# Kernel optimization log

Measured on AMD Instinct MI355X. Metric: run time of the kernel, lower is better.

Reference implementation:

```python
import math
import jax, jax.numpy as jnp
import numpy as np

B, N, D = 32, 1025, 768
K, CD, TD = 64, 128, 256  # num_clusters, cluster_dim, token_dim
REG = 0.1
NUM_ITERS = 5


def setup_inputs() -> dict:
    key = jax.random.key(0)
    ks = jax.random.split(key, 8)
    x = jax.random.normal(ks[0], (B, N, D), dtype=jnp.float32)
    # Linear params (torch nn.Linear: y = x @ W.T + b; we store W already transposed as [in, out])
    Wf = jax.random.normal(ks[1], (D, CD), dtype=jnp.float32) / math.sqrt(D)
    bf = jnp.zeros((CD,), dtype=jnp.float32)
    Ws = jax.random.normal(ks[2], (D, K), dtype=jnp.float32) / math.sqrt(D)
    bs = jnp.zeros((K,), dtype=jnp.float32)
    Wt = jax.random.normal(ks[3], (D, TD), dtype=jnp.float32) / math.sqrt(D)
    bt = jnp.zeros((TD,), dtype=jnp.float32)
    anchors = jax.random.normal(ks[4], (K, CD), dtype=jnp.float32) * 0.1
    dust_bin = jnp.float32(1.0)
    sharpness = jnp.float32(5.0)
    return {"x": x, "Wf": Wf, "bf": bf, "Ws": Ws, "bs": bs, "Wt": Wt, "bt": bt,
            "anchors": anchors, "dust_bin": dust_bin, "sharpness": sharpness}


def _log_otp_solver(log_a, log_b, M, num_iters, reg):
    M = M / reg
    u = jnp.zeros_like(log_a)  # [B, K+1]
    v = jnp.zeros_like(log_b)  # [B, N-1]
    for _ in range(num_iters):
        u = log_a - jax.nn.logsumexp(M + v[:, None, :], axis=2)
        v = log_b - jax.nn.logsumexp(M + u[:, :, None], axis=1)
    return M + u[:, :, None] + v[:, None, :]


def reference(x, Wf, bf, Ws, bs, Wt, bt, anchors, dust_bin, sharpness):
    b, n, d = x.shape
    t_global = x[:, 0]            # [B, D]
    fi = x[:, 1:]                 # [B, N-1, D]
    f = fi @ Wf + bf              # [B, N-1, CD]
    s = jnp.swapaxes(fi @ Ws + bs, 1, 2)  # [B, K, N-1]
    t = t_global @ Wt + bt        # [B, TD]
    s = s * sharpness
    dust = jnp.broadcast_to(dust_bin, (b, 1, n - 1))
    s_aug = jnp.concatenate([s, dust], axis=1)  # [B, K+1, N-1]
    log_a = jnp.full((b, K + 1), -math.log(K + 1), dtype=x.dtype)
    log_b = jnp.full((b, n - 1), -math.log(n - 1), dtype=x.dtype)
    log_P = _log_otp_solver(log_a, log_b, s_aug, NUM_ITERS, REG)
    p = jnp.exp(log_P)[:, :-1, :]  # [B, K, N-1]
    # v_agg = sum_n p[b,k,n] * (2*f[b,n,:] - anchors[k,:])  (algebraic rewrite of the broadcast sum)
    v_agg = 2.0 * jnp.einsum('bkn,bnc->bkc', p, f) - p.sum(axis=2)[:, :, None] * anchors[None]
    v_local = v_agg.reshape(b, -1)            # [B, K*CD]
    f_out = jnp.concatenate([t, v_local], axis=-1)
    norm = jnp.maximum(jnp.linalg.norm(f_out, axis=-1, keepdims=True), 1e-12)
    return f_out / norm
```

## Files before the change

### kernel.cpp

```cpp
#include <hip/hip_runtime.h>
#include <math.h>


#define BATCH 32
#define NTOK  1025
#define DIM   768
#define KDIM  64
#define CDIM  128
#define TDIM  256
#define NM1   1024
#define ROWLEN 8448
#define NITER 5
#define INV_REG 10.0f
#define NS_AGG 8
#define LOG_A (-4.17438727f)
#define LOG_B (-6.93147181f)

typedef __attribute__((ext_vector_type(8))) short short8;
typedef __attribute__((ext_vector_type(4))) float floatx4;

typedef __attribute__((address_space(3))) unsigned int lds_uint;
typedef const __attribute__((address_space(1))) unsigned int glb_uint;

__device__ __forceinline__ void gload_lds16(const void* g, void* l) {
    __builtin_amdgcn_global_load_lds((glb_uint*)g, (lds_uint*)l, 16, 0, 0);
}

__device__ __forceinline__ unsigned short bf16_rne(float f) {
    unsigned u = __builtin_bit_cast(unsigned, f);
    unsigned r = u + 0x7FFFu + ((u >> 16) & 1u);
    return (unsigned short)(r >> 16);
}

__device__ __forceinline__ short8 cvt8(float4 a, float4 b) {
    short8 r;
    r[0] = (short)bf16_rne(a.x); r[1] = (short)bf16_rne(a.y);
    r[2] = (short)bf16_rne(a.z); r[3] = (short)bf16_rne(a.w);
    r[4] = (short)bf16_rne(b.x); r[5] = (short)bf16_rne(b.y);
    r[6] = (short)bf16_rne(b.z); r[7] = (short)bf16_rne(b.w);
    return r;
}

__global__ __launch_bounds__(256) void prep(
    const float* __restrict__ Wf, const float* __restrict__ Ws,
    const float* __restrict__ bf, const float* __restrict__ bs,
    const float* __restrict__ x, const float* __restrict__ Wt,
    short* __restrict__ W_pack, float* __restrict__ bias_all,
    float* __restrict__ tpart)
{
    __shared__ float xr[256];
    const int blk = blockIdx.x, tid = threadIdx.x;
    if (blk < 576) {
        int idx = blk * 256 + tid;
        int g    = idx / 6144;
        int rem  = idx - g * 6144;
        int nf   = rem >> 9;
        int rem2 = rem & 511;
        int lane = rem2 >> 3;
        int j    = rem2 & 7;
        int k = g * 32 + (lane >> 4) * 8 + j;
        int c = nf * 16 + (lane & 15);
        float v = (c < CDIM) ? Wf[(size_t)k * CDIM + c] : Ws[(size_t)k * KDIM + (c - CDIM)];
        W_pack[idx] = (short)bf16_rne(v);
        if (idx < 192) bias_all[idx] = (idx < CDIM) ? bf[idx] : bs[idx - CDIM];
    } else {
        int i = blk - 576;
        int b = i / 3, dy = i - b * 3;
        xr[tid] = x[(size_t)b * NTOK * DIM + (size_t)dy * 256 + tid];
        __syncthreads();
        float acc = 0.f;
        const float* wp = Wt + (size_t)dy * 256 * TDIM + tid;
#pragma unroll 8
        for (int d = 0; d < 256; ++d) acc = fmaf(xr[d], wp[(size_t)d * TDIM], acc);
        tpart[((size_t)dy * BATCH + b) * TDIM + tid] = acc;
    }
}

__global__ __launch_bounds__(256, 2) void gemm_fs(
    const float* __restrict__ x, const short* __restrict__ W_pack,
    const float* __restrict__ bias_all, const float* __restrict__ sharp_p,
    unsigned short* __restrict__ fT, float* __restrict__ Mmat)
{
    __shared__ __align__(16) short Bs[12288];
    __shared__ __align__(16) short As[4096];
    const int tid  = threadIdx.x;
    const int wave = tid >> 6, lane = tid & 63;
    const int quad = lane >> 4, lrow = lane & 15;
    const int bb0   = blockIdx.x & 31;
    const int chunk = blockIdx.x >> 5;
    const int R = bb0 * 1024 + chunk * 64 + wave * 16;

    const int arow = bb0 * 1024 + chunk * 64 + (tid >> 2);
    const float* asrc = x + ((size_t)(arow >> 10) * NTOK + 1 + (arow & 1023)) * DIM + (tid & 3) * 16;
    const int r    = (tid >> 2) & 15;
    const int seg  = tid & 3;
    const int kk_w = seg >> 1;
    const int q0   = (seg & 1) * 2;
    short* adst0 = &As[(((tid >> 6) * 2 + kk_w) * 64 + q0 * 16 + r) * 8];
    short* adst1 = &As[(((tid >> 6) * 2 + kk_w) * 64 + (q0 + 1) * 16 + r) * 8];

    floatx4 acc[12];
#pragma unroll
    for (int nf = 0; nf < 12; ++nf) acc[nf] = (floatx4){0.f, 0.f, 0.f, 0.f};

    float4 g0 = *(const float4*)(asrc);
    float4 g1 = *(const float4*)(asrc + 4);
    float4 g2 = *(const float4*)(asrc + 8);
    float4 g3 = *(const float4*)(asrc + 12);

    for (int ko = 0; ko < 12; ++ko) {
        __syncthreads();
        const short* bsrc = W_pack + ko * 12288 + tid * 8;
#pragma unroll
        for (int i = 0; i < 6; ++i)
            gload_lds16(bsrc + i * 2048, &Bs[i * 2048 + tid * 8]);
        *(short8*)adst0 = cvt8(g0, g1);
        *(short8*)adst1 = cvt8(g2, g3);
        if (ko < 11) {
            const float* ap = asrc + (ko + 1) * 64;
            g0 = *(const float4*)(ap);
            g1 = *(const float4*)(ap + 4);
            g2 = *(const float4*)(ap + 8);
            g3 = *(const float4*)(ap + 12);
        }
        __syncthreads();
#pragma unroll
        for (int kk = 0; kk < 2; ++kk) {
            short8 af = *(const short8*)&As[((wave * 2 + kk) * 64 + lane) * 8];
#pragma unroll
            for (int nf = 0; nf < 12; ++nf) {
                short8 bf8 = *(const short8*)&Bs[((kk * 12 + nf) * 64 + lane) * 8];
                acc[nf] = __builtin_amdgcn_mfma_f32_16x16x32_bf16(af, bf8, acc[nf], 0, 0, 0);
            }
        }
    }

    const float sc = sharp_p[0] * INV_REG;
    const int bb = R >> 10;
    const int tok = (R & 1023) + quad * 4;
#pragma unroll
    for (int nf = 0; nf < 12; ++nf) {
        const int c = nf * 16 + lrow;
        const float bias = bias_all[c];
        if (nf < 8) {
            ushort4 w;
            w.x = bf16_rne(acc[nf][0] + bias);
            w.y = bf16_rne(acc[nf][1] + bias);
            w.z = bf16_rne(acc[nf][2] + bias);
            w.w = bf16_rne(acc[nf][3] + bias);
            *(ushort4*)(fT + ((size_t)bb * CDIM + c) * NM1 + tok) = w;
        } else {
            const int k = c - CDIM;
            float4 w = make_float4((acc[nf][0] + bias) * sc, (acc[nf][1] + bias) * sc,
                                   (acc[nf][2] + bias) * sc, (acc[nf][3] + bias) * sc);
            *(float4*)(Mmat + ((size_t)bb * KDIM + k) * NM1 + tok) = w;
        }
    }
}

template<bool FIRST>
__global__ __launch_bounds__(256) void sink_u(
    const float* __restrict__ Mmat, const float* __restrict__ v_in,
    const float* __restrict__ dust_p, float* __restrict__ u_out)
{
    const int b   = blockIdx.x & 31;
    const int sub = blockIdx.x >> 5;
    const int k   = sub * 4 + (threadIdx.x >> 6);
    if (k > 64) return;
    const int lane = threadIdx.x & 63;
    const float dustM = dust_p[0] * INV_REG;

    const float4* vp = (const float4*)(v_in + (size_t)b * NM1);
    float xs[16];
    if (k < 64) {
        const float4* Mp = (const float4*)(Mmat + ((size_t)b * KDIM + k) * NM1);
#pragma unroll
        for (int i = 0; i < 4; ++i) {
            float4 mv = Mp[i * 64 + lane];
            float4 vv = FIRST ? make_float4(0.f, 0.f, 0.f, 0.f) : vp[i * 64 + lane];
            xs[i * 4 + 0] = mv.x + vv.x;
            xs[i * 4 + 1] = mv.y + vv.y;
            xs[i * 4 + 2] = mv.z + vv.z;
            xs[i * 4 + 3] = mv.w + vv.w;
        }
    } else {
#pragma unroll
        for (int i = 0; i < 4; ++i) {
            float4 vv = FIRST ? make_float4(0.f, 0.f, 0.f, 0.f) : vp[i * 64 + lane];
            xs[i * 4 + 0] = dustM + vv.x;
            xs[i * 4 + 1] = dustM + vv.y;
            xs[i * 4 + 2] = dustM + vv.z;
            xs[i * 4 + 3] = dustM + vv.w;
        }
    }
    float m = xs[0];
#pragma unroll
    for (int i = 1; i < 16; ++i) m = fmaxf(m, xs[i]);
#pragma unroll
    for (int off = 1; off < 64; off <<= 1) m = fmaxf(m, __shfl_xor(m, off));
    float S = 0.f;
#pragma unroll
    for (int i = 0; i < 16; ++i) S += __expf(xs[i] - m);
#pragma unroll
    for (int off = 1; off < 64; off <<= 1) S += __shfl_xor(S, off);
    if (lane == 0) u_out[b * 65 + k] = LOG_A - (m + __logf(S));
}

__global__ __launch_bounds__(256) void sink_v(
    const float* __restrict__ Mmat, const float* __restrict__ u_in,
    const float* __restrict__ dust_p, float* __restrict__ v_out)
{
    __shared__ float us[65];
    __shared__ float2 pp[4][64];
    const int b   = blockIdx.x & 31;
    const int ns2 = blockIdx.x >> 5;
    const int tid = threadIdx.x;
    const int tok = tid & 63, kq = tid >> 6;
    const int n = ns2 * 64 + tok;
    if (tid < 65) us[tid] = u_in[b * 65 + tid];
    __syncthreads();
    const float* Mb = Mmat + ((size_t)b * KDIM + kq * 16) * NM1 + n;
    float xs[16];
#pragma unroll
    for (int kk = 0; kk < 16; ++kk) xs[kk] = Mb[(size_t)kk * NM1] + us[kq * 16 + kk];
    float m = xs[0];
#pragma unroll
    for (int kk = 1; kk < 16; ++kk) m = fmaxf(m, xs[kk]);
    float e = 0.f;
#pragma unroll
    for (int kk = 0; kk < 16; ++kk) e += __expf(xs[kk] - m);
    pp[kq][tok] = make_float2(m, e);
    __syncthreads();
    if (tid < 64) {
        const float xd = dust_p[0] * INV_REG + us[64];
        float m3 = xd;
#pragma unroll
        for (int q = 0; q < 4; ++q) m3 = fmaxf(m3, pp[q][tid].x);
        float S3 = __expf(xd - m3);
#pragma unroll
        for (int q = 0; q < 4; ++q) S3 += pp[q][tid].y * __expf(pp[q][tid].x - m3);
        v_out[(size_t)b * NM1 + ns2 * 64 + tid] = LOG_B - (m3 + __logf(S3));
    }
}

__global__ __launch_bounds__(256) void aggregate(
    const float* __restrict__ Mmat, const unsigned short* __restrict__ fT,
    const float* __restrict__ u_in, const float* __restrict__ dust_p,
    float* __restrict__ vpart, float* __restrict__ rspart)
{
    __shared__ float us[65];
    __shared__ __align__(16) float vsh[128];
    __shared__ float wv[4][128][2];
    const int b = blockIdx.x, ns = blockIdx.y;
    const int tid = threadIdx.x;
    const int wave = tid >> 6, lane = tid & 63;
    const int quad = lane >> 4, lrow = lane & 15;
    const int krow = wave * 16 + lrow;
    const float dustM = dust_p[0] * INV_REG;

    if (tid < 65) us[tid] = u_in[b * 65 + tid];
    __syncthreads();

    float mreg[32];
    {
        const float* Mrow = Mmat + ((size_t)b * KDIM + krow) * NM1 + ns * 128 + quad * 8;
#pragma unroll
        for (int s = 0; s < 4; ++s) {
            float4 a = *(const float4*)(Mrow + s * 32);
            float4 c = *(const float4*)(Mrow + s * 32 + 4);
            mreg[s*8+0]=a.x; mreg[s*8+1]=a.y; mreg[s*8+2]=a.z; mreg[s*8+3]=a.w;
            mreg[s*8+4]=c.x; mreg[s*8+5]=c.y; mreg[s*8+6]=c.z; mreg[s*8+7]=c.w;
        }
    }

    const float uk = us[krow];
#pragma unroll
    for (int s = 0; s < 4; ++s) {
#pragma unroll
        for (int j = 0; j < 8; ++j) {
            float x = mreg[s*8+j] + uk;
            float m2 = x;
            m2 = fmaxf(m2, __shfl_xor(m2, 1));
            m2 = fmaxf(m2, __shfl_xor(m2, 2));
            m2 = fmaxf(m2, __shfl_xor(m2, 4));
            m2 = fmaxf(m2, __shfl_xor(m2, 8));
            float e = __expf(x - m2);
            e += __shfl_xor(e, 1);
            e += __shfl_xor(e, 2);
            e += __shfl_xor(e, 4);
            e += __shfl_xor(e, 8);
            if (lrow == 0) {
                wv[wave][s*32 + quad*8 + j][0] = m2;
                wv[wave][s*32 + quad*8 + j][1] = e;
            }
        }
    }
    __syncthreads();
    if (tid < 128) {
        const float xd = dustM + us[64];
        float m3 = xd;
#pragma unroll
        for (int w = 0; w < 4; ++w) m3 = fmaxf(m3, wv[w][tid][0]);
        float S3 = __expf(xd - m3);
#pragma unroll
        for (int w = 0; w < 4; ++w) S3 += wv[w][tid][1] * __expf(wv[w][tid][0] - m3);
        vsh[tid] = LOG_B - (m3 + __logf(S3));
    }
    __syncthreads();

    const unsigned short* fbase = fT + ((size_t)b * CDIM + lrow) * NM1 + ns * 128 + quad * 8;
    floatx4 acc[8];
#pragma unroll
    for (int nf = 0; nf < 8; ++nf) acc[nf] = (floatx4){0.f, 0.f, 0.f, 0.f};
    float rs = 0.f;
#pragma unroll
    for (int s = 0; s < 4; ++s) {
        const int tb = s * 32 + quad * 8;
        float4 v0 = *(const float4*)&vsh[tb];
        float4 v1 = *(const float4*)&vsh[tb + 4];
        float p[8];
        p[0] = __expf(mreg[s*8+0] + uk + v0.x);
        p[1] = __expf(mreg[s*8+1] + uk + v0.y);
        p[2] = __expf(mreg[s*8+2] + uk + v0.z);
        p[3] = __expf(mreg[s*8+3] + uk + v0.w);
        p[4] = __expf(mreg[s*8+4] + uk + v1.x);
        p[5] = __expf(mreg[s*8+5] + uk + v1.y);
        p[6] = __expf(mreg[s*8+6] + uk + v1.z);
        p[7] = __expf(mreg[s*8+7] + uk + v1.w);
        short8 afrag;
#pragma unroll
        for (int j = 0; j < 8; ++j) {
            rs += p[j];
            afrag[j] = (short)bf16_rne(p[j]);
        }
#pragma unroll
        for (int nf = 0; nf < 8; ++nf) {
            short8 bfrag = *(const short8*)(fbase + (size_t)nf * 16 * NM1 + s * 32);
            acc[nf] = __builtin_amdgcn_mfma_f32_16x16x32_bf16(afrag, bfrag, acc[nf], 0, 0, 0);
        }
    }
    rs += __shfl_xor(rs, 16);
    rs += __shfl_xor(rs, 32);
    if (lane < 16) rspart[(ns * BATCH + b) * KDIM + krow] = rs;

    float* vp = vpart + (size_t)(ns * BATCH + b) * (KDIM * CDIM);
#pragma unroll
    for (int nf = 0; nf < 8; ++nf) {
        const int c = nf * 16 + lrow;
#pragma unroll
        for (int j = 0; j < 4; ++j)
            vp[(size_t)(wave * 16 + quad * 4 + j) * CDIM + c] = acc[nf][j];
    }
}

__global__ __launch_bounds__(1024) void finalize_all(
    const float* __restrict__ vpart, const float* __restrict__ rspart,
    const float* __restrict__ anchors, const float* __restrict__ tpart,
    const float* __restrict__ bt, float* __restrict__ out)
{
    __shared__ float rstot[KDIM];
    __shared__ float red[16];
    __shared__ float sc_sh;
    const int b = blockIdx.x, tid = threadIdx.x;
    const int lane = tid & 63, wave = tid >> 6;

    if (tid < KDIM) {
        float s = 0.f;
#pragma unroll
        for (int ns = 0; ns < NS_AGG; ++ns)
            s += rspart[(ns * BATCH + b) * KDIM + tid];
        rstot[tid] = s;
    }
    __syncthreads();

    const size_t e0 = (size_t)tid * 8;
    float4 s0 = make_float4(0.f, 0.f, 0.f, 0.f);
    float4 s1 = make_float4(0.f, 0.f, 0.f, 0.f);
#pragma unroll
    for (int ns = 0; ns < NS_AGG; ++ns) {
        const float* vp = vpart + (size_t)(ns * BATCH + b) * (KDIM * CDIM) + e0;
        float4 a = *(const float4*)(vp);
        float4 c = *(const float4*)(vp + 4);
        s0.x += a.x; s0.y += a.y; s0.z += a.z; s0.w += a.w;
        s1.x += c.x; s1.y += c.y; s1.z += c.z; s1.w += c.w;
    }
    const float rsv = rstot[tid >> 4];
    float4 a0 = *(const float4*)(anchors + e0);
    float4 a1 = *(const float4*)(anchors + e0 + 4);
    float4 v0, v1;
    v0.x = 2.f * s0.x - rsv * a0.x;  v0.y = 2.f * s0.y - rsv * a0.y;
    v0.z = 2.f * s0.z - rsv * a0.z;  v0.w = 2.f * s0.w - rsv * a0.w;
    v1.x = 2.f * s1.x - rsv * a1.x;  v1.y = 2.f * s1.y - rsv * a1.y;
    v1.z = 2.f * s1.z - rsv * a1.z;  v1.w = 2.f * s1.w - rsv * a1.w;
    float ss = v0.x*v0.x + v0.y*v0.y + v0.z*v0.z + v0.w*v0.w
             + v1.x*v1.x + v1.y*v1.y + v1.z*v1.z + v1.w*v1.w;

    float t = 0.f;
    if (tid < TDIM) {
        t = bt[tid];
#pragma unroll
        for (int s = 0; s < 3; ++s) t += tpart[((size_t)s * BATCH + b) * TDIM + tid];
        ss += t * t;
    }

#pragma unroll
    for (int off = 32; off > 0; off >>= 1) ss += __shfl_down(ss, off);
    if (lane == 0) red[wave] = ss;
    __syncthreads();
    if (tid == 0) {
        float tot = 0.f;
#pragma unroll
        for (int i = 0; i < 16; ++i) tot += red[i];
        sc_sh = 1.f / fmaxf(sqrtf(tot), 1e-12f);
    }
    __syncthreads();
    const float scale = sc_sh;

    float* orow = out + (size_t)b * ROWLEN;
    if (tid < TDIM) orow[tid] = t * scale;
    v0.x *= scale; v0.y *= scale; v0.z *= scale; v0.w *= scale;
    v1.x *= scale; v1.y *= scale; v1.z *= scale; v1.w *= scale;
    *(float4*)&orow[TDIM + e0]     = v0;
    *(float4*)&orow[TDIM + e0 + 4] = v1;
}

extern "C" void kernel_launch(void* const* d_in, const int* in_sizes, int n_in,
                              void* d_out, int out_size, void* d_ws, size_t ws_size,
                              hipStream_t stream)
{
    const float* x       = (const float*)d_in[0];
    const float* Wf      = (const float*)d_in[1];
    const float* bf      = (const float*)d_in[2];
    const float* Ws      = (const float*)d_in[3];
    const float* bs      = (const float*)d_in[4];
    const float* Wt      = (const float*)d_in[5];
    const float* bt      = (const float*)d_in[6];
    const float* anchors = (const float*)d_in[7];
    const float* dust    = (const float*)d_in[8];
    const float* sharp   = (const float*)d_in[9];
    float* out = (float*)d_out;

    char* base = (char*)d_ws;
    short* W_pack        = (short*)base;
    float* bias_all      = (float*)(base + 294912);
    float* Mmat          = bias_all + 192;
    unsigned short* fT   = (unsigned short*)(Mmat + (size_t)BATCH * KDIM * NM1);
    float* u_buf         = (float*)(fT + (size_t)BATCH * CDIM * NM1);
    float* v_buf         = u_buf + BATCH * 65;
    float* vpart         = v_buf + BATCH * NM1;
    float* rspart        = vpart + (size_t)NS_AGG * BATCH * KDIM * CDIM;
    float* tpart         = rspart + NS_AGG * BATCH * KDIM;

    hipLaunchKernelGGL(prep, dim3(672), dim3(256), 0, stream,
                       Wf, Ws, bf, bs, x, Wt, W_pack, bias_all, tpart);
    hipLaunchKernelGGL(gemm_fs, dim3(512), dim3(256), 0, stream,
                       x, W_pack, bias_all, sharp, fT, Mmat);

    hipLaunchKernelGGL(HIP_KERNEL_NAME(sink_u<true>), dim3(544), dim3(256), 0, stream,
                       Mmat, v_buf, dust, u_buf);
    for (int it = 1; it < NITER; ++it) {
        hipLaunchKernelGGL(sink_v, dim3(512), dim3(256), 0, stream,
                           Mmat, u_buf, dust, v_buf);
        hipLaunchKernelGGL(HIP_KERNEL_NAME(sink_u<false>), dim3(544), dim3(256), 0, stream,
                           Mmat, v_buf, dust, u_buf);
    }

    hipLaunchKernelGGL(aggregate, dim3(BATCH, NS_AGG), dim3(256), 0, stream,
                       Mmat, fT, u_buf, dust, vpart, rspart);
    hipLaunchKernelGGL(finalize_all, dim3(BATCH), dim3(1024), 0, stream,
                       vpart, rspart, anchors, tpart, bt, out);
}
```

Before: 245.5 us.

## Fuse Sinkhorn u/v half-steps into split-reduction kernels with partial logsumexp

Replaces the alternating sink_u/sink_v kernels with a single sink_uv kernel per iteration. Each block computes v for its token slice and then emits partial (max, sum) pairs for the next u update, and the consumer combines them. The first u partials are produced in the gemm_fs epilogue, and aggregate now merges the final partials itself. This cuts the launch count from about 10 to 4 plus aggregate and avoids re-reading Mmat twice per iteration. The cost is some extra reduction work, and it relies on a correct partial-logsumexp merge that treats the dust row specially.

```diff
diff --git a/kernel.cpp b/kernel.cpp
--- a/kernel.cpp
+++ b/kernel.cpp
@@ -79,10 +79,12 @@
 __global__ __launch_bounds__(256, 2) void gemm_fs(
     const float* __restrict__ x, const short* __restrict__ W_pack,
     const float* __restrict__ bias_all, const float* __restrict__ sharp_p,
-    unsigned short* __restrict__ fT, float* __restrict__ Mmat)
+    unsigned short* __restrict__ fT, float* __restrict__ Mmat,
+    float2* __restrict__ part0)
 {
     __shared__ __align__(16) short Bs[12288];
     __shared__ __align__(16) short As[4096];
+    __shared__ float2 sm[4][4][16];
     const int tid  = threadIdx.x;
     const int wave = tid >> 6, lane = tid & 63;
     const int quad = lane >> 4, lrow = lane & 15;
@@ -154,113 +156,50 @@
             float4 w = make_float4((acc[nf][0] + bias) * sc, (acc[nf][1] + bias) * sc,
                                    (acc[nf][2] + bias) * sc, (acc[nf][3] + bias) * sc);
             *(float4*)(Mmat + ((size_t)bb * KDIM + k) * NM1 + tok) = w;
-        }
-    }
-}
-
-template<bool FIRST>
-__global__ __launch_bounds__(256) void sink_u(
-    const float* __restrict__ Mmat, const float* __restrict__ v_in,
-    const float* __restrict__ dust_p, float* __restrict__ u_out)
-{
-    const int b   = blockIdx.x & 31;
-    const int sub = blockIdx.x >> 5;
-    const int k   = sub * 4 + (threadIdx.x >> 6);
-    if (k > 64) return;
-    const int lane = threadIdx.x & 63;
-    const float dustM = dust_p[0] * INV_REG;
-
-    const float4* vp = (const float4*)(v_in + (size_t)b * NM1);
-    float xs[16];
-    if (k < 64) {
-        const float4* Mp = (const float4*)(Mmat + ((size_t)b * KDIM + k) * NM1);
-#pragma unroll
-        for (int i = 0; i < 4; ++i) {
-            float4 mv = Mp[i * 64 + lane];
-            float4 vv = FIRST ? make_float4(0.f, 0.f, 0.f, 0.f) : vp[i * 64 + lane];
-            xs[i * 4 + 0] = mv.x + vv.x;
-            xs[i * 4 + 1] = mv.y + vv.y;
-            xs[i * 4 + 2] = mv.z + vv.z;
-            xs[i * 4 + 3] = mv.w + vv.w;
-        }
-    } else {
-#pragma unroll
-        for (int i = 0; i < 4; ++i) {
-            float4 vv = FIRST ? make_float4(0.f, 0.f, 0.f, 0.f) : vp[i * 64 + lane];
-            xs[i * 4 + 0] = dustM + vv.x;
-            xs[i * 4 + 1] = dustM + vv.y;
-            xs[i * 4 + 2] = dustM + vv.z;
-            xs[i * 4 + 3] = dustM + vv.w;
-        }
-    }
-    float m = xs[0];
-#pragma unroll
-    for (int i = 1; i < 16; ++i) m = fmaxf(m, xs[i]);
-#pragma unroll
-    for (int off = 1; off < 64; off <<= 1) m = fmaxf(m, __shfl_xor(m, off));
-    float S = 0.f;
-#pragma unroll
-    for (int i = 0; i < 16; ++i) S += __expf(xs[i] - m);
-#pragma unroll
-    for (int off = 1; off < 64; off <<= 1) S += __shfl_xor(S, off);
-    if (lane == 0) u_out[b * 65 + k] = LOG_A - (m + __logf(S));
-}
-
-__global__ __launch_bounds__(256) void sink_v(
-    const float* __restrict__ Mmat, const float* __restrict__ u_in,
-    const float* __restrict__ dust_p, float* __restrict__ v_out)
-{
-    __shared__ float us[65];
-    __shared__ float2 pp[4][64];
-    const int b   = blockIdx.x & 31;
-    const int ns2 = blockIdx.x >> 5;
-    const int tid = threadIdx.x;
-    const int tok = tid & 63, kq = tid >> 6;
-    const int n = ns2 * 64 + tok;
-    if (tid < 65) us[tid] = u_in[b * 65 + tid];
-    __syncthreads();
-    const float* Mb = Mmat + ((size_t)b * KDIM + kq * 16) * NM1 + n;
-    float xs[16];
-#pragma unroll
-    for (int kk = 0; kk < 16; ++kk) xs[kk] = Mb[(size_t)kk * NM1] + us[kq * 16 + kk];
-    float m = xs[0];
-#pragma unroll
-    for (int kk = 1; kk < 16; ++kk) m = fmaxf(m, xs[kk]);
-    float e = 0.f;
-#pragma unroll
-    for (int kk = 0; kk < 16; ++kk) e += __expf(xs[kk] - m);
-    pp[kq][tok] = make_float2(m, e);
-    __syncthreads();
-    if (tid < 64) {
-        const float xd = dust_p[0] * INV_REG + us[64];
-        float m3 = xd;
-#pragma unroll
-        for (int q = 0; q < 4; ++q) m3 = fmaxf(m3, pp[q][tid].x);
-        float S3 = __expf(xd - m3);
-#pragma unroll
-        for (int q = 0; q < 4; ++q) S3 += pp[q][tid].y * __expf(pp[q][tid].x - m3);
-        v_out[(size_t)b * NM1 + ns2 * 64 + tid] = LOG_B - (m3 + __logf(S3));
-    }
-}
-
-__global__ __launch_bounds__(256) void aggregate(
-    const float* __restrict__ Mmat, const unsigned short* __restrict__ fT,
-    const float* __restrict__ u_in, const float* __restrict__ dust_p,
-    float* __restrict__ vpart, float* __restrict__ rspart)
+            float m = fmaxf(fmaxf(w.x, w.y), fmaxf(w.z, w.w));
+            m = fmaxf(m, __shfl_xor(m, 16));
+            m = fmaxf(m, __shfl_xor(m, 32));
+            float e = __expf(w.x - m) + __expf(w.y - m)
+                    + __expf(w.z - m) + __expf(w.w - m);
+            e += __shfl_xor(e, 16);
+            e += __shfl_xor(e, 32);
+            if (quad == 0) sm[wave][nf - 8][lrow] = make_float2(m, e);
+        }
+    }
+    __syncthreads();
+    if (tid < 65) {
+        float2 o;
+        if (tid < 64) {
+            float2 p0 = sm[0][tid >> 4][tid & 15];
+            float2 p1 = sm[1][tid >> 4][tid & 15];
+            float2 p2 = sm[2][tid >> 4][tid & 15];
+            float2 p3 = sm[3][tid >> 4][tid & 15];
+            float m = fmaxf(fmaxf(p0.x, p1.x), fmaxf(p2.x, p3.x));
+            float e = p0.y * __expf(p0.x - m) + p1.y * __expf(p1.x - m)
+                    + p2.y * __expf(p2.x - m) + p3.y * __expf(p3.x - m);
+            o = make_float2(m, e);
+        } else {
+            o = make_float2(0.f, 64.f);
+        }
+        part0[((size_t)bb0 * 16 + chunk) * 65 + tid] = o;
+    }
+}
+
+template<int NSIN>
+__global__ __launch_bounds__(256) void sink_uv(
+    const float* __restrict__ Mmat, const float* __restrict__ dust_p,
+    const float2* __restrict__ pin, float2* __restrict__ pout)
 {
     __shared__ float us[65];
     __shared__ __align__(16) float vsh[128];
     __shared__ float wv[4][128][2];
-    const int b = blockIdx.x, ns = blockIdx.y;
+    const int b = blockIdx.x & 31, ns = blockIdx.x >> 5;
     const int tid = threadIdx.x;
     const int wave = tid >> 6, lane = tid & 63;
     const int quad = lane >> 4, lrow = lane & 15;
     const int krow = wave * 16 + lrow;
     const float dustM = dust_p[0] * INV_REG;
 
-    if (tid < 65) us[tid] = u_in[b * 65 + tid];
-    __syncthreads();
-
     float mreg[32];
     {
         const float* Mrow = Mmat + ((size_t)b * KDIM + krow) * NM1 + ns * 128 + quad * 8;
@@ -272,6 +211,19 @@
             mreg[s*8+4]=c.x; mreg[s*8+5]=c.y; mreg[s*8+6]=c.z; mreg[s*8+7]=c.w;
         }
     }
+
+    if (tid < 65) {
+        const float2* pr = pin + (size_t)b * NSIN * 65 + tid;
+        float M2 = -3.4e38f;
+        float2 pv[NSIN];
+#pragma unroll
+        for (int q = 0; q < NSIN; ++q) { pv[q] = pr[q * 65]; M2 = fmaxf(M2, pv[q].x); }
+        float S2 = 0.f;
+#pragma unroll
+        for (int q = 0; q < NSIN; ++q) S2 += pv[q].y * __expf(pv[q].x - M2);
+        us[tid] = LOG_A - (M2 + __logf(S2));
+    }
+    __syncthreads();
 
     const float uk = us[krow];
 #pragma unroll
@@ -308,6 +260,116 @@
     }
     __syncthreads();
 
+    float xs[32];
+#pragma unroll
+    for (int s = 0; s < 4; ++s) {
+        const int tb = s * 32 + quad * 8;
+        float4 v0 = *(const float4*)&vsh[tb];
+        float4 v1 = *(const float4*)&vsh[tb + 4];
+        xs[s*8+0]=mreg[s*8+0]+v0.x; xs[s*8+1]=mreg[s*8+1]+v0.y;
+        xs[s*8+2]=mreg[s*8+2]+v0.z; xs[s*8+3]=mreg[s*8+3]+v0.w;
+        xs[s*8+4]=mreg[s*8+4]+v1.x; xs[s*8+5]=mreg[s*8+5]+v1.y;
+        xs[s*8+6]=mreg[s*8+6]+v1.z; xs[s*8+7]=mreg[s*8+7]+v1.w;
+    }
+    float mx = xs[0];
+#pragma unroll
+    for (int i = 1; i < 32; ++i) mx = fmaxf(mx, xs[i]);
+    mx = fmaxf(mx, __shfl_xor(mx, 16));
+    mx = fmaxf(mx, __shfl_xor(mx, 32));
+    float S = 0.f;
+#pragma unroll
+    for (int i = 0; i < 32; ++i) S += __expf(xs[i] - mx);
+    S += __shfl_xor(S, 16);
+    S += __shfl_xor(S, 32);
+    float2* pb = pout + ((size_t)b * NS_AGG + ns) * 65;
+    if (quad == 0) pb[krow] = make_float2(mx, S);
+    if (wave == 0) {
+        float v0 = vsh[lane], v1 = vsh[64 + lane];
+        float md = fmaxf(v0, v1);
+#pragma unroll
+        for (int off = 1; off < 64; off <<= 1) md = fmaxf(md, __shfl_xor(md, off));
+        float Sd = __expf(v0 - md) + __expf(v1 - md);
+#pragma unroll
+        for (int off = 1; off < 64; off <<= 1) Sd += __shfl_xor(Sd, off);
+        if (lane == 0) pb[64] = make_float2(dustM + md, Sd);
+    }
+}
+
+__global__ __launch_bounds__(256) void aggregate(
+    const float* __restrict__ Mmat, const unsigned short* __restrict__ fT,
+    const float2* __restrict__ pin, const float* __restrict__ dust_p,
+    float* __restrict__ vpart, float* __restrict__ rspart)
+{
+    __shared__ float us[65];
+    __shared__ __align__(16) float vsh[128];
+    __shared__ float wv[4][128][2];
+    const int b = blockIdx.x & 31, ns = blockIdx.x >> 5;
+    const int tid = threadIdx.x;
+    const int wave = tid >> 6, lane = tid & 63;
+    const int quad = lane >> 4, lrow = lane & 15;
+    const int krow = wave * 16 + lrow;
+    const float dustM = dust_p[0] * INV_REG;
+
+    float mreg[32];
+    {
+        const float* Mrow = Mmat + ((size_t)b * KDIM + krow) * NM1 + ns * 128 + quad * 8;
+#pragma unroll
+        for (int s = 0; s < 4; ++s) {
+            float4 a = *(const float4*)(Mrow + s * 32);
+            float4 c = *(const float4*)(Mrow + s * 32 + 4);
+            mreg[s*8+0]=a.x; mreg[s*8+1]=a.y; mreg[s*8+2]=a.z; mreg[s*8+3]=a.w;
+            mreg[s*8+4]=c.x; mreg[s*8+5]=c.y; mreg[s*8+6]=c.z; mreg[s*8+7]=c.w;
+        }
+    }
+
+    if (tid < 65) {
+        const float2* pr = pin + (size_t)b * NS_AGG * 65 + tid;
+        float2 pv[8];
+        float M2 = -3.4e38f;
+#pragma unroll
+        for (int q = 0; q < 8; ++q) { pv[q] = pr[q * 65]; M2 = fmaxf(M2, pv[q].x); }
+        float S2 = 0.f;
+#pragma unroll
+        for (int q = 0; q < 8; ++q) S2 += pv[q].y * __expf(pv[q].x - M2);
+        us[tid] = LOG_A - (M2 + __logf(S2));
+    }
+    __syncthreads();
+
+    const float uk = us[krow];
+#pragma unroll
+    for (int s = 0; s < 4; ++s) {
+#pragma unroll
+        for (int j = 0; j < 8; ++j) {
+            float x = mreg[s*8+j] + uk;
+            float m2 = x;
+            m2 = fmaxf(m2, __shfl_xor(m2, 1));
+            m2 = fmaxf(m2, __shfl_xor(m2, 2));
+            m2 = fmaxf(m2, __shfl_xor(m2, 4));
+            m2 = fmaxf(m2, __shfl_xor(m2, 8));
+            float e = __expf(x - m2);
+            e += __shfl_xor(e, 1);
+            e += __shfl_xor(e, 2);
+            e += __shfl_xor(e, 4);
+            e += __shfl_xor(e, 8);
+            if (lrow == 0) {
+                wv[wave][s*32 + quad*8 + j][0] = m2;
+                wv[wave][s*32 + quad*8 + j][1] = e;
+            }
+        }
+    }
+    __syncthreads();
+    if (tid < 128) {
+        const float xd = dustM + us[64];
+        float m3 = xd;
+#pragma unroll
+        for (int w = 0; w < 4; ++w) m3 = fmaxf(m3, wv[w][tid][0]);
+        float S3 = __expf(xd - m3);
+#pragma unroll
+        for (int w = 0; w < 4; ++w) S3 += wv[w][tid][1] * __expf(wv[w][tid][0] - m3);
+        vsh[tid] = LOG_B - (m3 + __logf(S3));
+    }
+    __syncthreads();
+
     const unsigned short* fbase = fT + ((size_t)b * CDIM + lrow) * NM1 + ns * 128 + quad * 8;
     floatx4 acc[8];
 #pragma unroll
@@ -445,28 +507,29 @@
     float* bias_all      = (float*)(base + 294912);
     float* Mmat          = bias_all + 192;
     unsigned short* fT   = (unsigned short*)(Mmat + (size_t)BATCH * KDIM * NM1);
-    float* u_buf         = (float*)(fT + (size_t)BATCH * CDIM * NM1);
-    float* v_buf         = u_buf + BATCH * 65;
-    float* vpart         = v_buf + BATCH * NM1;
+    float2* part0        = (float2*)(fT + (size_t)BATCH * CDIM * NM1);
+    float2* partA        = part0 + (size_t)BATCH * 16 * 65;
+    float2* partB        = partA + (size_t)BATCH * 8 * 65;
+    float* vpart         = (float*)(partB + (size_t)BATCH * 8 * 65);
     float* rspart        = vpart + (size_t)NS_AGG * BATCH * KDIM * CDIM;
     float* tpart         = rspart + NS_AGG * BATCH * KDIM;
 
     hipLaunchKernelGGL(prep, dim3(672), dim3(256), 0, stream,
                        Wf, Ws, bf, bs, x, Wt, W_pack, bias_all, tpart);
     hipLaunchKernelGGL(gemm_fs, dim3(512), dim3(256), 0, stream,
-                       x, W_pack, bias_all, sharp, fT, Mmat);
-
-    hipLaunchKernelGGL(HIP_KERNEL_NAME(sink_u<true>), dim3(544), dim3(256), 0, stream,
-                       Mmat, v_buf, dust, u_buf);
-    for (int it = 1; it < NITER; ++it) {
-        hipLaunchKernelGGL(sink_v, dim3(512), dim3(256), 0, stream,
-                           Mmat, u_buf, dust, v_buf);
-        hipLaunchKernelGGL(HIP_KERNEL_NAME(sink_u<false>), dim3(544), dim3(256), 0, stream,
-                           Mmat, v_buf, dust, u_buf);
-    }
-
-    hipLaunchKernelGGL(aggregate, dim3(BATCH, NS_AGG), dim3(256), 0, stream,
-                       Mmat, fT, u_buf, dust, vpart, rspart);
+                       x, W_pack, bias_all, sharp, fT, Mmat, part0);
+
+    hipLaunchKernelGGL(HIP_KERNEL_NAME(sink_uv<16>), dim3(256), dim3(256), 0, stream,
+                       Mmat, dust, part0, partA);
+    hipLaunchKernelGGL(HIP_KERNEL_NAME(sink_uv<8>), dim3(256), dim3(256), 0, stream,
+                       Mmat, dust, partA, partB);
+    hipLaunchKernelGGL(HIP_KERNEL_NAME(sink_uv<8>), dim3(256), dim3(256), 0, stream,
+                       Mmat, dust, partB, partA);
+    hipLaunchKernelGGL(HIP_KERNEL_NAME(sink_uv<8>), dim3(256), dim3(256), 0, stream,
+                       Mmat, dust, partA, partB);
+
+    hipLaunchKernelGGL(aggregate, dim3(256), dim3(256), 0, stream,
+                       Mmat, fT, partB, dust, vpart, rspart);
     hipLaunchKernelGGL(finalize_all, dim3(BATCH), dim3(1024), 0, stream,
                        vpart, rspart, anchors, tpart, bt, out);
 }
```

After: 266.0 us. 8.4% more time.
